# Performance work log

Hardware: AMD Instinct MI355X
Metric: run time of the kernel (lower is better)

The kernel has to match this reference:

```python
import jax, jax.numpy as jnp
import numpy as np

N_NODES = 10000
N_EDGES = 320000
N_GRAPHS = 64
K = 10
IN_C, HID_C, OUT_C = 128, 256, 128


def setup_inputs() -> dict:
    key = jax.random.key(0)
    ks = jax.random.split(key, 10)
    s_in = 1.0 / np.sqrt(IN_C)
    s_hid = 1.0 / np.sqrt(HID_C)
    return {
        "x": jax.random.normal(ks[0], (N_NODES, IN_C), jnp.float32),
        "W0": jax.random.normal(ks[1], (K, IN_C, HID_C), jnp.float32) * s_in,
        "b0": jnp.zeros((HID_C,), jnp.float32),
        "W1": jax.random.normal(ks[2], (K, HID_C, HID_C), jnp.float32) * s_hid,
        "b1": jnp.zeros((HID_C,), jnp.float32),
        "W2": jax.random.normal(ks[3], (K, HID_C, HID_C), jnp.float32) * s_hid,
        "b2": jnp.zeros((HID_C,), jnp.float32),
        "W_out": jax.random.normal(ks[4], (HID_C, OUT_C), jnp.float32) * s_hid,
        "b_out": jnp.zeros((OUT_C,), jnp.float32),
        "edge_index": jax.random.randint(ks[5], (2, N_EDGES), 0, N_NODES, jnp.int64),
        "batch": jnp.sort(jax.random.randint(ks[6], (N_NODES,), 0, N_GRAPHS, jnp.int64)),
    }


def _edge_norm(src, dst, n):
    # Scaled Laplacian L_hat = 2L/lambda_max - I with lambda_max=2 and sym norm
    # => L_hat = -D^{-1/2} A D^{-1/2} (diagonal entries cancel to 0).
    deg = jnp.zeros((n,), jnp.float32).at[src].add(1.0)
    dis = jnp.where(deg > 0, jax.lax.rsqrt(jnp.maximum(deg, 1.0)), 0.0)
    return -dis[src] * dis[dst]


def _propagate(x, src, dst, w, n):
    # message = w * x[src], aggregated by sum at dst
    return jax.ops.segment_sum(w[:, None] * x[src], dst, num_segments=n)


def _cheb_conv(x, src, dst, w, W, b, n):
    # Tx_0 = x; Tx_1 = L_hat x; Tx_k = 2 L_hat Tx_{k-1} - Tx_{k-2}
    K_ = W.shape[0]
    Tx0 = x
    out = Tx0 @ W[0]
    Tx1 = _propagate(Tx0, src, dst, w, n)
    out = out + Tx1 @ W[1]
    for k in range(2, K_):
        Tx2 = 2.0 * _propagate(Tx1, src, dst, w, n) - Tx0
        out = out + Tx2 @ W[k]
        Tx0, Tx1 = Tx1, Tx2
    return out + b


def reference(x, W0, b0, W1, b1, W2, b2, W_out, b_out, edge_index, batch):
    n = x.shape[0]
    src, dst = edge_index[0], edge_index[1]
    w = _edge_norm(src, dst, n)
    # 3 ChebConv layers, each followed by ReLU (norm=None, dropout=0)
    h = jax.nn.relu(_cheb_conv(x, src, dst, w, W0, b0, n))
    h = jax.nn.relu(_cheb_conv(h, src, dst, w, W1, b1, n))
    h = jax.nn.relu(_cheb_conv(h, src, dst, w, W2, b2, n))
    # global_mean_pool over batch ids
    sums = jax.ops.segment_sum(h, batch, num_segments=N_GRAPHS)
    cnts = jax.ops.segment_sum(jnp.ones((n,), h.dtype), batch, num_segments=N_GRAPHS)
    pooled = sums / jnp.maximum(cnts, 1.0)[:, None]
    return pooled @ W_out + b_out
```

## Files before the change

### kernel.cpp

```cpp
#include <hip/hip_runtime.h>
#include <cstdint>
#include <cstddef>

#define N_NODES 10000
#define N_EDGES 320000
#define N_GRAPHS 64
#define KCHEB 10
#define C_IN 128
#define C_HID 256
#define C_OUTC 128
#define POOL_CHUNK 40

static inline size_t align_up(size_t v, size_t a){ return (v + a - 1) / a * a; }

typedef __attribute__((ext_vector_type(8))) _Float16 half8;
typedef __attribute__((ext_vector_type(2))) _Float16 h2;
typedef __attribute__((ext_vector_type(4))) float f32x4;


__global__ void k_deg(const int* __restrict__ src, const int* __restrict__ dst,
                      int* __restrict__ deg, int* __restrict__ indeg){
  int e = blockIdx.x*blockDim.x + threadIdx.x;
  if(e < N_EDGES){
    atomicAdd(&deg[src[e]], 1);
    atomicAdd(&indeg[dst[e]], 1);
  }
}

__global__ void k_dis(const int* __restrict__ deg, float* __restrict__ dis){
  int i = blockIdx.x*blockDim.x + threadIdx.x;
  if(i < N_NODES){
    int d = deg[i];
    dis[i] = d > 0 ? rsqrtf((float)d) : 0.f;
  }
}

__global__ void k_edgew(const int* __restrict__ src, const int* __restrict__ dst,
                        const float* __restrict__ dis, float* __restrict__ w){
  int e = blockIdx.x*blockDim.x + threadIdx.x;
  if(e < N_EDGES){
    w[e] = -dis[src[e]] * dis[dst[e]];
  }
}

__global__ __launch_bounds__(1024) void k_scan(const int* __restrict__ cnt,
                                               int* __restrict__ offs,
                                               int* __restrict__ cursor){
  __shared__ int part[1024];
  const int n = N_NODES;
  const int CH = (n + 1023) / 1024;
  int tid = threadIdx.x;
  int base = tid * CH;
  int s = 0;
  for(int i = 0; i < CH; i++){
    int idx = base + i;
    if(idx < n) s += cnt[idx];
  }
  part[tid] = s;
  __syncthreads();
  for(int off = 1; off < 1024; off <<= 1){
    int v = (tid >= off) ? part[tid - off] : 0;
    __syncthreads();
    part[tid] += v;
    __syncthreads();
  }
  int run = (tid == 0) ? 0 : part[tid - 1];
  for(int i = 0; i < CH; i++){
    int idx = base + i;
    if(idx < n){
      offs[idx] = run;
      cursor[idx] = run;
      run += cnt[idx];
    }
  }
  if(tid == 1023) offs[n] = part[1023];
}

__global__ void k_scatter(const int* __restrict__ src, const int* __restrict__ dst,
                          const float* __restrict__ w, int* __restrict__ cursor,
                          int* __restrict__ csr_s, float* __restrict__ csr_w){
  int e = blockIdx.x*blockDim.x + threadIdx.x;
  if(e < N_EDGES){
    int d = dst[e];
    int p = atomicAdd(&cursor[d], 1);
    csr_s[p] = src[e];
    csr_w[p] = w[e];
  }
}

__global__ __launch_bounds__(128) void k_gbounds(const int* __restrict__ batch,
                                                 int* __restrict__ gstart,
                                                 int* __restrict__ gcnt){
  int g = threadIdx.x;
  if(g <= N_GRAPHS){
    int lo = 0, hi = N_NODES;
    while(lo < hi){
      int mid = (lo + hi) >> 1;
      if(batch[mid] < g) lo = mid + 1; else hi = mid;
    }
    gstart[g] = lo;
  }
  __syncthreads();
  if(g < N_GRAPHS) gcnt[g] = gstart[g + 1] - gstart[g];
}


__device__ inline void hfma4(h2* a, uint4 v, unsigned wbits){
  h2 w2 = __builtin_bit_cast(h2, wbits);
  a[0] += __builtin_bit_cast(h2, v.x) * w2;
  a[1] += __builtin_bit_cast(h2, v.y) * w2;
  a[2] += __builtin_bit_cast(h2, v.z) * w2;
  a[3] += __builtin_bit_cast(h2, v.w) * w2;
}

__global__ __launch_bounds__(256) void k_prop256h(const _Float16* __restrict__ Xb,
                                                  const _Float16* __restrict__ Pb,
                                                  _Float16* __restrict__ tx,
                                                  const int* __restrict__ csr_s,
                                                  const float* __restrict__ csr_w,
                                                  const int* __restrict__ offs,
                                                  float alpha){
  const int stride  = KCHEB * C_HID;
  const int strideB = stride * 2;
  int bid  = blockIdx.x;
  int half = (bid >> 2) & 1;
  int lh   = (bid >> 3) * 4 + (bid & 3);
  int l15  = threadIdx.x & 15;
  int lane = threadIdx.x & 63;
  int b16  = lane & 48;
  int node = lh * 16 + (threadIdx.x >> 4);
  if(node >= N_NODES) return;
  int j0 = offs[node], j1 = offs[node + 1];
  h2 a[4] = {};
  const char* __restrict__ gbase = (const char*)Xb + (half * (C_HID/2) + l15 * 8) * 2;
  int j = j0;
  int sv = 0; unsigned wv = 0;
  bool have = (j + 7 < j1);
  if(have){
    sv = csr_s[j + (l15 & 7)] * strideB;
    unsigned short wb = __builtin_bit_cast(unsigned short, (_Float16)csr_w[j + (l15 & 7)]);
    wv = (unsigned)wb * 0x00010001u;
  }
  while(have){
    int jn = j + 8;
    bool more = (jn + 7 < j1);
    int sv2 = 0; unsigned wv2 = 0;
    if(more){
      sv2 = csr_s[jn + (l15 & 7)] * strideB;
      unsigned short wb = __builtin_bit_cast(unsigned short, (_Float16)csr_w[jn + (l15 & 7)]);
      wv2 = (unsigned)wb * 0x00010001u;
    }
    uint4 v[8];
#pragma unroll
    for(int i = 0; i < 8; i++){
      int si = __shfl(sv, b16 + i);
      v[i] = *(const uint4*)(gbase + si);
    }
#pragma unroll
    for(int i = 0; i < 8; i++){
      unsigned wi = (unsigned)__shfl((int)wv, b16 + i);
      hfma4(a, v[i], wi);
    }
    sv = sv2; wv = wv2; j = jn; have = more;
  }
  for(; j < j1; j++){
    int si = csr_s[j] * strideB;
    unsigned short wb = __builtin_bit_cast(unsigned short, (_Float16)csr_w[j]);
    unsigned wi = (unsigned)wb * 0x00010001u;
    uint4 v0 = *(const uint4*)(gbase + si);
    hfma4(a, v0, wi);
  }
  _Float16 ah = (_Float16)alpha;
  h2 al = {ah, ah};
  h2 r[4];
#pragma unroll
  for(int i = 0; i < 4; i++) r[i] = a[i] * al;
  size_t off = (size_t)node * stride + half * (C_HID/2) + l15 * 8;
  if(Pb){
    uint4 pv = *(const uint4*)(Pb + off);
    r[0] -= __builtin_bit_cast(h2, pv.x);
    r[1] -= __builtin_bit_cast(h2, pv.y);
    r[2] -= __builtin_bit_cast(h2, pv.z);
    r[3] -= __builtin_bit_cast(h2, pv.w);
  }
  uint4 ob;
  ob.x = __builtin_bit_cast(unsigned, r[0]);
  ob.y = __builtin_bit_cast(unsigned, r[1]);
  ob.z = __builtin_bit_cast(unsigned, r[2]);
  ob.w = __builtin_bit_cast(unsigned, r[3]);
  *(uint4*)(tx + off) = ob;
}

__global__ __launch_bounds__(256) void k_prop128(const _Float16* __restrict__ Xb,
                                                 const _Float16* __restrict__ Pb,
                                                 _Float16* __restrict__ tx,
                                                 const int* __restrict__ csr_s,
                                                 const float* __restrict__ csr_w,
                                                 const int* __restrict__ offs,
                                                 float alpha){
  const int stride  = KCHEB * C_IN;
  const int strideB = stride * 2;
  int hl   = threadIdx.x & 31;
  int b32  = threadIdx.x & 32;
  int node = blockIdx.x * 8 + (threadIdx.x >> 5);
  int j0 = offs[node], j1 = offs[node + 1];
  h2 a[2] = {};
  const char* __restrict__ gbase = (const char*)Xb + hl * 8;
  int j = j0;
  int sv = 0; unsigned wv = 0;
  bool have = (j + 7 < j1);
  if(have){
    sv = csr_s[j + (hl & 7)] * strideB;
    unsigned short wb = __builtin_bit_cast(unsigned short, (_Float16)csr_w[j + (hl & 7)]);
    wv = (unsigned)wb * 0x00010001u;
  }
  while(have){
    int jn = j + 8;
    bool more = (jn + 7 < j1);
    int sv2 = 0; unsigned wv2 = 0;
    if(more){
      sv2 = csr_s[jn + (hl & 7)] * strideB;
      unsigned short wb = __builtin_bit_cast(unsigned short, (_Float16)csr_w[jn + (hl & 7)]);
      wv2 = (unsigned)wb * 0x00010001u;
    }
    uint2 v[8];
#pragma unroll
    for(int i = 0; i < 8; i++){
      int si = __shfl(sv, b32 + i);
      v[i] = *(const uint2*)(gbase + si);
    }
#pragma unroll
    for(int i = 0; i < 8; i++){
      unsigned wi = (unsigned)__shfl((int)wv, b32 + i);
      h2 w2 = __builtin_bit_cast(h2, wi);
      a[0] += __builtin_bit_cast(h2, v[i].x) * w2;
      a[1] += __builtin_bit_cast(h2, v[i].y) * w2;
    }
    sv = sv2; wv = wv2; j = jn; have = more;
  }
  for(; j < j1; j++){
    int si = csr_s[j] * strideB;
    unsigned short wb = __builtin_bit_cast(unsigned short, (_Float16)csr_w[j]);
    h2 w2 = __builtin_bit_cast(h2, (unsigned)wb * 0x00010001u);
    uint2 v0 = *(const uint2*)(gbase + si);
    a[0] += __builtin_bit_cast(h2, v0.x) * w2;
    a[1] += __builtin_bit_cast(h2, v0.y) * w2;
  }
  _Float16 ah = (_Float16)alpha;
  h2 al = {ah, ah};
  h2 r0 = a[0] * al, r1 = a[1] * al;
  size_t off = (size_t)node * stride + hl * 4;
  if(Pb){
    uint2 pv = *(const uint2*)(Pb + off);
    r0 -= __builtin_bit_cast(h2, pv.x);
    r1 -= __builtin_bit_cast(h2, pv.y);
  }
  uint2 ob;
  ob.x = __builtin_bit_cast(unsigned, r0);
  ob.y = __builtin_bit_cast(unsigned, r1);
  *(uint2*)(tx + off) = ob;
}

template<int C>
__global__ void k_f2h(const float* __restrict__ X, _Float16* __restrict__ tx,
                      int tx_stride){
  int idx = blockIdx.x * blockDim.x + threadIdx.x;
  const int GPR = C / 4;
  if(idx < N_NODES * GPR){
    int r = idx / GPR;
    int c = (idx - r * GPR) * 4;
    float4 v = *(const float4*)(X + (size_t)r * C + c);
    h2 p0 = {(_Float16)v.x, (_Float16)v.y};
    h2 p1 = {(_Float16)v.z, (_Float16)v.w};
    uint2 ob;
    ob.x = __builtin_bit_cast(unsigned, p0);
    ob.y = __builtin_bit_cast(unsigned, p1);
    *(uint2*)(tx + (size_t)r * tx_stride + c) = ob;
  }
}

__global__ void k_wt3(const float* __restrict__ W0, _Float16* __restrict__ WT0,
                      const float* __restrict__ W1, _Float16* __restrict__ WT1,
                      const float* __restrict__ W2, _Float16* __restrict__ WT2){
  const int n0 = KCHEB * C_IN  * C_HID;
  const int n1 = KCHEB * C_HID * C_HID;
  int idx = blockIdx.x * blockDim.x + threadIdx.x;
  if(idx < n0){
    int Ktot = KCHEB * C_IN;
    int o = idx / Ktot, kc = idx - o * Ktot;
    WT0[idx] = (_Float16)W0[(size_t)kc * 256 + o];
  } else if(idx < n0 + n1){
    int i = idx - n0;
    int Ktot = KCHEB * C_HID;
    int o = i / Ktot, kc = i - o * Ktot;
    WT1[i] = (_Float16)W1[(size_t)kc * 256 + o];
  } else if(idx < n0 + 2 * n1){
    int i = idx - n0 - n1;
    int Ktot = KCHEB * C_HID;
    int o = i / Ktot, kc = i - o * Ktot;
    WT2[i] = (_Float16)W2[(size_t)kc * 256 + o];
  }
}


__global__ __launch_bounds__(256) void k_gemm_f(const _Float16* __restrict__ A,
                                                const _Float16* __restrict__ BT,
                                                const float* __restrict__ bias,
                                                float* __restrict__ H,
                                                _Float16* __restrict__ tx2,
                                                int M, int Ktot){
  int b = blockIdx.x;
  int xcd = b & 7;
  int l = b >> 3;
  int m = xcd + 8 * (l >> 2);
  int n = l & 3;
  if(m * 64 >= M) return;
  int row0 = m * 64, col0 = n * 64;

  __shared__ short As[2][64 * 64];
  __shared__ short Bs[2][64 * 64];
  int tid = threadIdx.x;
  int lane = tid & 63;
  int wave = tid >> 6;
  int l15 = lane & 15;
  int quad = lane >> 4;
  int wm = (wave & 1) * 32;
  int wn = (wave >> 1) * 32;

  int e0 = tid, e1 = tid + 256;
  int r0 = e0 >> 3, g0 = e0 & 7;
  int r1 = e1 >> 3, g1 = e1 & 7;
  int gr0 = row0 + r0, gr1 = row0 + r1;
  int sa0 = r0 * 64 + ((g0 ^ (r0 & 7)) * 8);
  int sa1 = r1 * 64 + ((g1 ^ (r1 & 7)) * 8);

  f32x4 acc[2][2] = {};
  uint4 av0, av1, bv0, bv1;

  auto load = [&](int k0){
    av0 = (gr0 < M) ? *(const uint4*)(A + (size_t)gr0 * Ktot + k0 + g0 * 8)
                    : make_uint4(0u, 0u, 0u, 0u);
    av1 = (gr1 < M) ? *(const uint4*)(A + (size_t)gr1 * Ktot + k0 + g1 * 8)
                    : make_uint4(0u, 0u, 0u, 0u);
    bv0 = *(const uint4*)(BT + (size_t)(col0 + r0) * Ktot + k0 + g0 * 8);
    bv1 = *(const uint4*)(BT + (size_t)(col0 + r1) * Ktot + k0 + g1 * 8);
  };
  auto stor = [&](int buf){
    *(uint4*)(&As[buf][sa0]) = av0;
    *(uint4*)(&As[buf][sa1]) = av1;
    *(uint4*)(&Bs[buf][sa0]) = bv0;
    *(uint4*)(&Bs[buf][sa1]) = bv1;
  };

  load(0);
  stor(0);
  __syncthreads();
  int nk = Ktot >> 6;
  for(int it = 0; it < nk; it++){
    int cur = it & 1;
    if(it + 1 < nk) load((it + 1) << 6);
#pragma unroll
    for(int kk = 0; kk < 64; kk += 32){
      int g = (kk >> 3) + quad;
      half8 a[2], bb[2];
#pragma unroll
      for(int mi = 0; mi < 2; mi++){
        int r = wm + mi * 16 + l15;
        a[mi] = *(const half8*)(&As[cur][r * 64 + ((g ^ (r & 7)) * 8)]);
      }
#pragma unroll
      for(int ni = 0; ni < 2; ni++){
        int nn = wn + ni * 16 + l15;
        bb[ni] = *(const half8*)(&Bs[cur][nn * 64 + ((g ^ (nn & 7)) * 8)]);
      }
#pragma unroll
      for(int mi = 0; mi < 2; mi++)
#pragma unroll
        for(int ni = 0; ni < 2; ni++)
          acc[mi][ni] = __builtin_amdgcn_mfma_f32_16x16x32_f16(a[mi], bb[ni], acc[mi][ni], 0, 0, 0);
    }
    if(it + 1 < nk){
      stor(cur ^ 1);
      __syncthreads();
    }
  }

  const int K256 = KCHEB * C_HID;
#pragma unroll
  for(int mi = 0; mi < 2; mi++){
#pragma unroll
    for(int ni = 0; ni < 2; ni++){
      int gcol = col0 + wn + ni * 16 + l15;
      float bv = bias[gcol];
#pragma unroll
      for(int r = 0; r < 4; r++){
        int grow = row0 + wm + mi * 16 + quad * 4 + r;
        if(grow < M){
          float v = fmaxf(acc[mi][ni][r] + bv, 0.f);
          if(tx2) tx2[(size_t)grow * K256 + gcol] = (_Float16)v;
          else    H[(size_t)grow * C_HID + gcol] = v;
        }
      }
    }
  }
}


__global__ __launch_bounds__(256) void k_pool2(const float* __restrict__ h,
                                               const int* __restrict__ batch,
                                               float* __restrict__ gsum){
  int c  = threadIdx.x;
  int n0 = blockIdx.x * POOL_CHUNK;
  int n1 = n0 + POOL_CHUNK;
  if(n1 > N_NODES) n1 = N_NODES;
  if(n0 >= n1) return;
  float acc = 0.f;
  int cur = batch[n0];
  for(int n = n0; n < n1; n++){
    int g = batch[n];
    if(g != cur){
      atomicAdd(&gsum[cur * C_HID + c], acc);
      acc = 0.f;
      cur = g;
    }
    acc += h[(size_t)n * C_HID + c];
  }
  atomicAdd(&gsum[cur * C_HID + c], acc);
}

__global__ __launch_bounds__(128) void k_final(const float* __restrict__ gsum,
                                               const int* __restrict__ gcnt,
                                               const float* __restrict__ Wout,
                                               const float* __restrict__ bout,
                                               float* __restrict__ out){
  int g = blockIdx.x;
  int o = threadIdx.x;
  float inv = 1.f / fmaxf((float)gcnt[g], 1.f);
  float acc = bout[o];
  for(int c = 0; c < C_HID; c++) acc += gsum[g * C_HID + c] * inv * Wout[c * C_OUTC + o];
  out[g * C_OUTC + o] = acc;
}


extern "C" void kernel_launch(void* const* d_in, const int* in_sizes, int n_in,
                              void* d_out, int out_size, void* d_ws, size_t ws_size,
                              hipStream_t stream){
  const float* x    = (const float*)d_in[0];
  const float* W0   = (const float*)d_in[1];
  const float* b0   = (const float*)d_in[2];
  const float* W1   = (const float*)d_in[3];
  const float* b1   = (const float*)d_in[4];
  const float* W2   = (const float*)d_in[5];
  const float* b2   = (const float*)d_in[6];
  const float* Wout = (const float*)d_in[7];
  const float* bout = (const float*)d_in[8];
  const int*   ei   = (const int*)d_in[9];
  const int*   batch= (const int*)d_in[10];
  const int* src = ei;
  const int* dst = ei + N_EDGES;
  float* out = (float*)d_out;

  char* p = (char*)d_ws;
  auto alloc = [&](size_t bytes)->char*{ char* r = p; p += align_up(bytes, 256); return r; };

  int*   deg    = (int*)  alloc(N_NODES * 4);
  int*   indeg  = (int*)  alloc(N_NODES * 4);
  int*   offs   = (int*)  alloc((N_NODES + 1) * 4);
  int*   cursor = (int*)  alloc(N_NODES * 4);
  float* dis    = (float*)alloc(N_NODES * 4);
  float* w_e    = (float*)alloc(N_EDGES * 4);
  int*   csr_s  = (int*)  alloc(N_EDGES * 4);
  float* csr_w  = (float*)alloc(N_EDGES * 4);
  int*   gcnt   = (int*)  alloc(N_GRAPHS * 4);
  int*   gstart = (int*)  alloc((N_GRAPHS + 1) * 4);
  float* gsum   = (float*)alloc(N_GRAPHS * C_HID * 4);

  const size_t txBytes = (size_t)N_NODES * (KCHEB * C_HID) * 2;
  _Float16* txP = (_Float16*)alloc(txBytes);
  _Float16* txQ = (_Float16*)alloc(txBytes);
  _Float16* WT0 = (_Float16*)alloc((size_t)KCHEB * C_IN  * C_HID * 2);
  _Float16* WT1 = (_Float16*)alloc((size_t)KCHEB * C_HID * C_HID * 2);
  _Float16* WT2 = (_Float16*)alloc((size_t)KCHEB * C_HID * C_HID * 2);
  float* Hb = (float*)alloc((size_t)N_NODES * C_HID * 4);

  hipMemsetAsync(deg,   0, N_NODES * 4, stream);
  hipMemsetAsync(indeg, 0, N_NODES * 4, stream);
  hipMemsetAsync(gsum,  0, N_GRAPHS * C_HID * 4, stream);

  const int TB = 256;
  int egrid = (N_EDGES + TB - 1) / TB;
  int ngrid = (N_NODES + TB - 1) / TB;

  k_deg<<<egrid, TB, 0, stream>>>(src, dst, deg, indeg);
  k_dis<<<ngrid, TB, 0, stream>>>(deg, dis);
  k_edgew<<<egrid, TB, 0, stream>>>(src, dst, dis, w_e);
  k_scan<<<1, 1024, 0, stream>>>(indeg, offs, cursor);
  k_scatter<<<egrid, TB, 0, stream>>>(src, dst, w_e, cursor, csr_s, csr_w);
  k_gbounds<<<1, 128, 0, stream>>>(batch, gstart, gcnt);

  {
    int ntot = KCHEB * C_IN * C_HID + 2 * KCHEB * C_HID * C_HID;
    k_wt3<<<(ntot + TB - 1) / TB, TB, 0, stream>>>(W0, WT0, W1, WT1, W2, WT2);
  }

  const int K128 = KCHEB * C_IN;
  const int K256 = KCHEB * C_HID;
  const int GEMM_BLOCKS = 640;
  const int PROP_H_BLOCKS = 1256;

  {
    int ng = N_NODES * (C_IN / 4);
    k_f2h<C_IN><<<(ng + TB - 1) / TB, TB, 0, stream>>>(x, txP, K128);
    for(int k = 1; k < KCHEB; k++){
      const _Float16* Xb = txP + (size_t)(k - 1) * C_IN;
      const _Float16* Pb = (k >= 2) ? txP + (size_t)(k - 2) * C_IN : nullptr;
      _Float16* tx = txP + (size_t)k * C_IN;
      k_prop128<<<N_NODES / 8, 256, 0, stream>>>(Xb, Pb, tx, csr_s, csr_w, offs,
                                                 k == 1 ? 1.f : 2.f);
    }
    k_gemm_f<<<GEMM_BLOCKS, 256, 0, stream>>>(txP, WT0, b0, nullptr, txQ, N_NODES, K128);
  }

  {
    for(int k = 1; k < KCHEB; k++){
      const _Float16* Xb = txQ + (size_t)(k - 1) * C_HID;
      const _Float16* Pb = (k >= 2) ? txQ + (size_t)(k - 2) * C_HID : nullptr;
      _Float16* tx = txQ + (size_t)k * C_HID;
      k_prop256h<<<PROP_H_BLOCKS, 256, 0, stream>>>(Xb, Pb, tx, csr_s, csr_w, offs,
                                                    k == 1 ? 1.f : 2.f);
    }
    k_gemm_f<<<GEMM_BLOCKS, 256, 0, stream>>>(txQ, WT1, b1, nullptr, txP, N_NODES, K256);
  }

  {
    for(int k = 1; k < KCHEB; k++){
      const _Float16* Xb = txP + (size_t)(k - 1) * C_HID;
      const _Float16* Pb = (k >= 2) ? txP + (size_t)(k - 2) * C_HID : nullptr;
      _Float16* tx = txP + (size_t)k * C_HID;
      k_prop256h<<<PROP_H_BLOCKS, 256, 0, stream>>>(Xb, Pb, tx, csr_s, csr_w, offs,
                                                    k == 1 ? 1.f : 2.f);
    }
    k_gemm_f<<<GEMM_BLOCKS, 256, 0, stream>>>(txP, WT2, b2, Hb, nullptr, N_NODES, K256);
  }

  k_pool2<<<(N_NODES + POOL_CHUNK - 1) / POOL_CHUNK, 256, 0, stream>>>(Hb, batch, gsum);
  k_final<<<N_GRAPHS, C_OUTC, 0, stream>>>(gsum, gcnt, Wout, bout, out);
}
```

Baseline: 642.4 us.

## Fuse edge-weight prep, prepack fp16 weights, tile weight transpose, enlarge GEMM tile

Folds the per-node inverse-sqrt degree into the scan kernel and computes edge weights inside the CSR scatter. The weights are stored there as packed half2 words, so the propagation kernels no longer convert them per edge and two small kernels are removed. The weight transpose now goes through a shared-memory tiled kernel to get coalesced reads and writes. The GEMM tile grows from 64 to 128 rows per block with half as many blocks, which raises reuse but also register and LDS use, and may lower occupancy.

```diff
diff --git a/kernel.cpp b/kernel.cpp
--- a/kernel.cpp
+++ b/kernel.cpp
@@ -27,25 +27,11 @@
   }
 }
 
-__global__ void k_dis(const int* __restrict__ deg, float* __restrict__ dis){
-  int i = blockIdx.x*blockDim.x + threadIdx.x;
-  if(i < N_NODES){
-    int d = deg[i];
-    dis[i] = d > 0 ? rsqrtf((float)d) : 0.f;
-  }
-}
-
-__global__ void k_edgew(const int* __restrict__ src, const int* __restrict__ dst,
-                        const float* __restrict__ dis, float* __restrict__ w){
-  int e = blockIdx.x*blockDim.x + threadIdx.x;
-  if(e < N_EDGES){
-    w[e] = -dis[src[e]] * dis[dst[e]];
-  }
-}
-
 __global__ __launch_bounds__(1024) void k_scan(const int* __restrict__ cnt,
                                                int* __restrict__ offs,
-                                               int* __restrict__ cursor){
+                                               int* __restrict__ cursor,
+                                               const int* __restrict__ deg,
+                                               float* __restrict__ dis){
   __shared__ int part[1024];
   const int n = N_NODES;
   const int CH = (n + 1023) / 1024;
@@ -54,7 +40,11 @@
   int s = 0;
   for(int i = 0; i < CH; i++){
     int idx = base + i;
-    if(idx < n) s += cnt[idx];
+    if(idx < n){
+      s += cnt[idx];
+      int d = deg[idx];
+      dis[idx] = d > 0 ? rsqrtf((float)d) : 0.f;
+    }
   }
   part[tid] = s;
   __syncthreads();
@@ -77,14 +67,16 @@
 }
 
 __global__ void k_scatter(const int* __restrict__ src, const int* __restrict__ dst,
-                          const float* __restrict__ w, int* __restrict__ cursor,
-                          int* __restrict__ csr_s, float* __restrict__ csr_w){
+                          const float* __restrict__ dis, int* __restrict__ cursor,
+                          int* __restrict__ csr_s, unsigned* __restrict__ csr_wp){
   int e = blockIdx.x*blockDim.x + threadIdx.x;
   if(e < N_EDGES){
-    int d = dst[e];
+    int s = src[e], d = dst[e];
+    float w = -dis[s] * dis[d];
+    unsigned short wb = __builtin_bit_cast(unsigned short, (_Float16)w);
     int p = atomicAdd(&cursor[d], 1);
-    csr_s[p] = src[e];
-    csr_w[p] = w[e];
+    csr_s[p] = s;
+    csr_wp[p] = (unsigned)wb * 0x00010001u;
   }
 }
 
@@ -117,7 +109,7 @@
                                                   const _Float16* __restrict__ Pb,
                                                   _Float16* __restrict__ tx,
                                                   const int* __restrict__ csr_s,
-                                                  const float* __restrict__ csr_w,
+                                                  const unsigned* __restrict__ csr_wp,
                                                   const int* __restrict__ offs,
                                                   float alpha){
   const int stride  = KCHEB * C_HID;
@@ -128,6 +120,7 @@
   int l15  = threadIdx.x & 15;
   int lane = threadIdx.x & 63;
   int b16  = lane & 48;
+  int e8   = l15 & 7;
   int node = lh * 16 + (threadIdx.x >> 4);
   if(node >= N_NODES) return;
   int j0 = offs[node], j1 = offs[node + 1];
@@ -136,20 +129,12 @@
   int j = j0;
   int sv = 0; unsigned wv = 0;
   bool have = (j + 7 < j1);
-  if(have){
-    sv = csr_s[j + (l15 & 7)] * strideB;
-    unsigned short wb = __builtin_bit_cast(unsigned short, (_Float16)csr_w[j + (l15 & 7)]);
-    wv = (unsigned)wb * 0x00010001u;
-  }
+  if(have){ sv = csr_s[j + e8] * strideB; wv = csr_wp[j + e8]; }
   while(have){
     int jn = j + 8;
     bool more = (jn + 7 < j1);
     int sv2 = 0; unsigned wv2 = 0;
-    if(more){
-      sv2 = csr_s[jn + (l15 & 7)] * strideB;
-      unsigned short wb = __builtin_bit_cast(unsigned short, (_Float16)csr_w[jn + (l15 & 7)]);
-      wv2 = (unsigned)wb * 0x00010001u;
-    }
+    if(more){ sv2 = csr_s[jn + e8] * strideB; wv2 = csr_wp[jn + e8]; }
     uint4 v[8];
 #pragma unroll
     for(int i = 0; i < 8; i++){
@@ -165,10 +150,8 @@
   }
   for(; j < j1; j++){
     int si = csr_s[j] * strideB;
-    unsigned short wb = __builtin_bit_cast(unsigned short, (_Float16)csr_w[j]);
-    unsigned wi = (unsigned)wb * 0x00010001u;
     uint4 v0 = *(const uint4*)(gbase + si);
-    hfma4(a, v0, wi);
+    hfma4(a, v0, csr_wp[j]);
   }
   _Float16 ah = (_Float16)alpha;
   h2 al = {ah, ah};
@@ -195,13 +178,14 @@
                                                  const _Float16* __restrict__ Pb,
                                                  _Float16* __restrict__ tx,
                                                  const int* __restrict__ csr_s,
-                                                 const float* __restrict__ csr_w,
+                                                 const unsigned* __restrict__ csr_wp,
                                                  const int* __restrict__ offs,
                                                  float alpha){
   const int stride  = KCHEB * C_IN;
   const int strideB = stride * 2;
   int hl   = threadIdx.x & 31;
   int b32  = threadIdx.x & 32;
+  int e8   = hl & 7;
   int node = blockIdx.x * 8 + (threadIdx.x >> 5);
   int j0 = offs[node], j1 = offs[node + 1];
   h2 a[2] = {};
@@ -209,20 +193,12 @@
   int j = j0;
   int sv = 0; unsigned wv = 0;
   bool have = (j + 7 < j1);
-  if(have){
-    sv = csr_s[j + (hl & 7)] * strideB;
-    unsigned short wb = __builtin_bit_cast(unsigned short, (_Float16)csr_w[j + (hl & 7)]);
-    wv = (unsigned)wb * 0x00010001u;
-  }
+  if(have){ sv = csr_s[j + e8] * strideB; wv = csr_wp[j + e8]; }
   while(have){
     int jn = j + 8;
     bool more = (jn + 7 < j1);
     int sv2 = 0; unsigned wv2 = 0;
-    if(more){
-      sv2 = csr_s[jn + (hl & 7)] * strideB;
-      unsigned short wb = __builtin_bit_cast(unsigned short, (_Float16)csr_w[jn + (hl & 7)]);
-      wv2 = (unsigned)wb * 0x00010001u;
-    }
+    if(more){ sv2 = csr_s[jn + e8] * strideB; wv2 = csr_wp[jn + e8]; }
     uint2 v[8];
 #pragma unroll
     for(int i = 0; i < 8; i++){
@@ -240,8 +216,7 @@
   }
   for(; j < j1; j++){
     int si = csr_s[j] * strideB;
-    unsigned short wb = __builtin_bit_cast(unsigned short, (_Float16)csr_w[j]);
-    h2 w2 = __builtin_bit_cast(h2, (unsigned)wb * 0x00010001u);
+    h2 w2 = __builtin_bit_cast(h2, csr_wp[j]);
     uint2 v0 = *(const uint2*)(gbase + si);
     a[0] += __builtin_bit_cast(h2, v0.x) * w2;
     a[1] += __builtin_bit_cast(h2, v0.y) * w2;
@@ -279,26 +254,27 @@
   }
 }
 
-__global__ void k_wt3(const float* __restrict__ W0, _Float16* __restrict__ WT0,
-                      const float* __restrict__ W1, _Float16* __restrict__ WT1,
-                      const float* __restrict__ W2, _Float16* __restrict__ WT2){
-  const int n0 = KCHEB * C_IN  * C_HID;
-  const int n1 = KCHEB * C_HID * C_HID;
-  int idx = blockIdx.x * blockDim.x + threadIdx.x;
-  if(idx < n0){
-    int Ktot = KCHEB * C_IN;
-    int o = idx / Ktot, kc = idx - o * Ktot;
-    WT0[idx] = (_Float16)W0[(size_t)kc * 256 + o];
-  } else if(idx < n0 + n1){
-    int i = idx - n0;
-    int Ktot = KCHEB * C_HID;
-    int o = i / Ktot, kc = i - o * Ktot;
-    WT1[i] = (_Float16)W1[(size_t)kc * 256 + o];
-  } else if(idx < n0 + 2 * n1){
-    int i = idx - n0 - n1;
-    int Ktot = KCHEB * C_HID;
-    int o = i / Ktot, kc = i - o * Ktot;
-    WT2[i] = (_Float16)W2[(size_t)kc * 256 + o];
+__global__ __launch_bounds__(256) void k_wt3t(const float* __restrict__ W0, _Float16* __restrict__ WT0,
+                                              const float* __restrict__ W1, _Float16* __restrict__ WT1,
+                                              const float* __restrict__ W2, _Float16* __restrict__ WT2){
+  __shared__ float t[32][33];
+  int b = blockIdx.x;
+  const float* W; _Float16* WT; int R; int tb;
+  if(b < 320){ W = W0; WT = WT0; R = 1280; tb = b; }
+  else if(b < 960){ W = W1; WT = WT1; R = 2560; tb = b - 320; }
+  else { W = W2; WT = WT2; R = 2560; tb = b - 960; }
+  int tr = tb >> 3, tc = tb & 7;
+  int tx = threadIdx.x & 31, ty = threadIdx.x >> 5;
+#pragma unroll
+  for(int i = 0; i < 4; i++){
+    int r = tr * 32 + ty + 8 * i;
+    t[ty + 8 * i][tx] = W[(size_t)r * 256 + tc * 32 + tx];
+  }
+  __syncthreads();
+#pragma unroll
+  for(int i = 0; i < 4; i++){
+    int o = tc * 32 + ty + 8 * i;
+    WT[(size_t)o * R + tr * 32 + tx] = (_Float16)t[tx][ty + 8 * i];
   }
 }
 
@@ -314,42 +290,52 @@
   int l = b >> 3;
   int m = xcd + 8 * (l >> 2);
   int n = l & 3;
-  if(m * 64 >= M) return;
-  int row0 = m * 64, col0 = n * 64;
-
-  __shared__ short As[2][64 * 64];
+  if(m * 128 >= M) return;
+  int row0 = m * 128, col0 = n * 64;
+
+  __shared__ short As[2][128 * 64];
   __shared__ short Bs[2][64 * 64];
   int tid = threadIdx.x;
   int lane = tid & 63;
   int wave = tid >> 6;
   int l15 = lane & 15;
   int quad = lane >> 4;
-  int wm = (wave & 1) * 32;
+  int wm = (wave & 1) * 64;
   int wn = (wave >> 1) * 32;
 
-  int e0 = tid, e1 = tid + 256;
-  int r0 = e0 >> 3, g0 = e0 & 7;
-  int r1 = e1 >> 3, g1 = e1 & 7;
-  int gr0 = row0 + r0, gr1 = row0 + r1;
-  int sa0 = r0 * 64 + ((g0 ^ (r0 & 7)) * 8);
-  int sa1 = r1 * 64 + ((g1 ^ (r1 & 7)) * 8);
-
-  f32x4 acc[2][2] = {};
-  uint4 av0, av1, bv0, bv1;
+  int ar[4], ag[4], asw[4], agr[4];
+#pragma unroll
+  for(int i = 0; i < 4; i++){
+    int e = tid + 256 * i;
+    ar[i] = e >> 3; ag[i] = e & 7;
+    agr[i] = row0 + ar[i];
+    asw[i] = ar[i] * 64 + ((ag[i] ^ (ar[i] & 7)) * 8);
+  }
+  int br[2], bg[2], bsw[2];
+#pragma unroll
+  for(int i = 0; i < 2; i++){
+    int e = tid + 256 * i;
+    br[i] = e >> 3; bg[i] = e & 7;
+    bsw[i] = br[i] * 64 + ((bg[i] ^ (br[i] & 7)) * 8);
+  }
+
+  f32x4 acc[4][2] = {};
+  uint4 av[4], bv[2];
 
   auto load = [&](int k0){
-    av0 = (gr0 < M) ? *(const uint4*)(A + (size_t)gr0 * Ktot + k0 + g0 * 8)
-                    : make_uint4(0u, 0u, 0u, 0u);
-    av1 = (gr1 < M) ? *(const uint4*)(A + (size_t)gr1 * Ktot + k0 + g1 * 8)
-                    : make_uint4(0u, 0u, 0u, 0u);
-    bv0 = *(const uint4*)(BT + (size_t)(col0 + r0) * Ktot + k0 + g0 * 8);
-    bv1 = *(const uint4*)(BT + (size_t)(col0 + r1) * Ktot + k0 + g1 * 8);
+#pragma unroll
+    for(int i = 0; i < 4; i++)
+      av[i] = (agr[i] < M) ? *(const uint4*)(A + (size_t)agr[i] * Ktot + k0 + ag[i] * 8)
+                           : make_uint4(0u, 0u, 0u, 0u);
+#pragma unroll
+    for(int i = 0; i < 2; i++)
+      bv[i] = *(const uint4*)(BT + (size_t)(col0 + br[i]) * Ktot + k0 + bg[i] * 8);
   };
   auto stor = [&](int buf){
-    *(uint4*)(&As[buf][sa0]) = av0;
-    *(uint4*)(&As[buf][sa1]) = av1;
-    *(uint4*)(&Bs[buf][sa0]) = bv0;
-    *(uint4*)(&Bs[buf][sa1]) = bv1;
+#pragma unroll
+    for(int i = 0; i < 4; i++) *(uint4*)(&As[buf][asw[i]]) = av[i];
+#pragma unroll
+    for(int i = 0; i < 2; i++) *(uint4*)(&Bs[buf][bsw[i]]) = bv[i];
   };
 
   load(0);
@@ -362,9 +348,9 @@
 #pragma unroll
     for(int kk = 0; kk < 64; kk += 32){
       int g = (kk >> 3) + quad;
-      half8 a[2], bb[2];
-#pragma unroll
-      for(int mi = 0; mi < 2; mi++){
+      half8 a[4], bb[2];
+#pragma unroll
+      for(int mi = 0; mi < 4; mi++){
         int r = wm + mi * 16 + l15;
         a[mi] = *(const half8*)(&As[cur][r * 64 + ((g ^ (r & 7)) * 8)]);
       }
@@ -374,7 +360,7 @@
         bb[ni] = *(const half8*)(&Bs[cur][nn * 64 + ((g ^ (nn & 7)) * 8)]);
       }
 #pragma unroll
-      for(int mi = 0; mi < 2; mi++)
+      for(int mi = 0; mi < 4; mi++)
 #pragma unroll
         for(int ni = 0; ni < 2; ni++)
           acc[mi][ni] = __builtin_amdgcn_mfma_f32_16x16x32_f16(a[mi], bb[ni], acc[mi][ni], 0, 0, 0);
@@ -387,16 +373,16 @@
 
   const int K256 = KCHEB * C_HID;
 #pragma unroll
-  for(int mi = 0; mi < 2; mi++){
+  for(int mi = 0; mi < 4; mi++){
 #pragma unroll
     for(int ni = 0; ni < 2; ni++){
       int gcol = col0 + wn + ni * 16 + l15;
-      float bv = bias[gcol];
+      float bvv = bias[gcol];
 #pragma unroll
       for(int r = 0; r < 4; r++){
         int grow = row0 + wm + mi * 16 + quad * 4 + r;
         if(grow < M){
-          float v = fmaxf(acc[mi][ni][r] + bv, 0.f);
+          float v = fmaxf(acc[mi][ni][r] + bvv, 0.f);
           if(tx2) tx2[(size_t)grow * K256 + gcol] = (_Float16)v;
           else    H[(size_t)grow * C_HID + gcol] = v;
         }
@@ -468,9 +454,8 @@
   int*   offs   = (int*)  alloc((N_NODES + 1) * 4);
   int*   cursor = (int*)  alloc(N_NODES * 4);
   float* dis    = (float*)alloc(N_NODES * 4);
-  float* w_e    = (float*)alloc(N_EDGES * 4);
   int*   csr_s  = (int*)  alloc(N_EDGES * 4);
-  float* csr_w  = (float*)alloc(N_EDGES * 4);
+  unsigned* csr_wp = (unsigned*)alloc(N_EDGES * 4);
   int*   gcnt   = (int*)  alloc(N_GRAPHS * 4);
   int*   gstart = (int*)  alloc((N_GRAPHS + 1) * 4);
   float* gsum   = (float*)alloc(N_GRAPHS * C_HID * 4);
@@ -489,24 +474,18 @@
 
   const int TB = 256;
   int egrid = (N_EDGES + TB - 1) / TB;
-  int ngrid = (N_NODES + TB - 1) / TB;
 
   k_deg<<<egrid, TB, 0, stream>>>(src, dst, deg, indeg);
-  k_dis<<<ngrid, TB, 0, stream>>>(deg, dis);
-  k_edgew<<<egrid, TB, 0, stream>>>(src, dst, dis, w_e);
-  k_scan<<<1, 1024, 0, stream>>>(indeg, offs, cursor);
-  k_scatter<<<egrid, TB, 0, stream>>>(src, dst, w_e, cursor, csr_s, csr_w);
+  k_scan<<<1, 1024, 0, stream>>>(indeg, offs, cursor, deg, dis);
+  k_scatter<<<egrid, TB, 0, stream>>>(src, dst, dis, cursor, csr_s, csr_wp);
   k_gbounds<<<1, 128, 0, stream>>>(batch, gstart, gcnt);
-
-  {
-    int ntot = KCHEB * C_IN * C_HID + 2 * KCHEB * C_HID * C_HID;
-    k_wt3<<<(ntot + TB - 1) / TB, TB, 0, stream>>>(W0, WT0, W1, WT1, W2, WT2);
-  }
+  k_wt3t<<<1600, 256, 0, stream>>>(W0, WT0, W1, WT1, W2, WT2);
 
   const int K128 = KCHEB * C_IN;
   const int K256 = KCHEB * C_HID;
-  const int GEMM_BLOCKS = 640;
+  const int GEMM_BLOCKS = 320;
   const int PROP_H_BLOCKS = 1256;
+  const int PROP_1_BLOCKS = N_NODES / 8;
 
   {
     int ng = N_NODES * (C_IN / 4);
@@ -515,8 +494,8 @@
       const _Float16* Xb = txP + (size_t)(k - 1) * C_IN;
       const _Float16* Pb = (k >= 2) ? txP + (size_t)(k - 2) * C_IN : nullptr;
       _Float16* tx = txP + (size_t)k * C_IN;
-      k_prop128<<<N_NODES / 8, 256, 0, stream>>>(Xb, Pb, tx, csr_s, csr_w, offs,
-                                                 k == 1 ? 1.f : 2.f);
+      k_prop128<<<PROP_1_BLOCKS, 256, 0, stream>>>(Xb, Pb, tx, csr_s, csr_wp, offs,
+                                                   k == 1 ? 1.f : 2.f);
     }
     k_gemm_f<<<GEMM_BLOCKS, 256, 0, stream>>>(txP, WT0, b0, nullptr, txQ, N_NODES, K128);
   }
@@ -526,7 +505,7 @@
       const _Float16* Xb = txQ + (size_t)(k - 1) * C_HID;
       const _Float16* Pb = (k >= 2) ? txQ + (size_t)(k - 2) * C_HID : nullptr;
       _Float16* tx = txQ + (size_t)k * C_HID;
-      k_prop256h<<<PROP_H_BLOCKS, 256, 0, stream>>>(Xb, Pb, tx, csr_s, csr_w, offs,
+      k_prop256h<<<PROP_H_BLOCKS, 256, 0, stream>>>(Xb, Pb, tx, csr_s, csr_wp, offs,
                                                     k == 1 ? 1.f : 2.f);
     }
     k_gemm_f<<<GEMM_BLOCKS, 256, 0, stream>>>(txQ, WT1, b1, nullptr, txP, N_NODES, K256);
@@ -537,7 +516,7 @@
       const _Float16* Xb = txP + (size_t)(k - 1) * C_HID;
       const _Float16* Pb = (k >= 2) ? txP + (size_t)(k - 2) * C_HID : nullptr;
       _Float16* tx = txP + (size_t)k * C_HID;
-      k_prop256h<<<PROP_H_BLOCKS, 256, 0, stream>>>(Xb, Pb, tx, csr_s, csr_w, offs,
+      k_prop256h<<<PROP_H_BLOCKS, 256, 0, stream>>>(Xb, Pb, tx, csr_s, csr_wp, offs,
                                                     k == 1 ? 1.f : 2.f);
     }
     k_gemm_f<<<GEMM_BLOCKS, 256, 0, stream>>>(txP, WT2, b2, Hb, nullptr, N_NODES, K256);
```

New measurement: 722.1 us. 1.12x slower.
